# Kernel optimization log

Hardware: AMD Instinct MI355X
Metric: run time of the kernel (lower is better)

## Reference

```python
import jax, jax.numpy as jnp
import numpy as np

N_P = 50000   # number of 'place' nodes
N_A = 50000   # number of 'a_transition' nodes
E = 1600000   # edges per edge type
IN = 128      # input feature dim
OUT = 64      # HANConv out_channels
H = 4         # heads
D = OUT // H  # per-head dim
HID = 64      # decoder hidden
NEG_SLOPE = 0.2  # HANConv leaky_relu slope


def setup_inputs() -> dict:
    key = jax.random.key(0)
    ks = jax.random.split(key, 24)
    def nrm(i, shape, scale=1.0):
        return jax.random.normal(ks[i], shape, dtype=jnp.float32) * scale
    w = lambda i, shape, fan: nrm(i, shape, (1.0 / fan) ** 0.5)
    return {
        "x_place": nrm(0, (N_P, IN)),
        "x_atrans": nrm(1, (N_A, IN)),
        "e_pa_src": jax.random.randint(ks[2], (E,), 0, N_P),
        "e_pa_dst": jax.random.randint(ks[3], (E,), 0, N_A),
        "e_aa_src": jax.random.randint(ks[4], (E,), 0, N_A),
        "e_aa_dst": jax.random.randint(ks[5], (E,), 0, N_A),
        "e_ap_src": jax.random.randint(ks[6], (E,), 0, N_A),
        "e_ap_dst": jax.random.randint(ks[7], (E,), 0, N_P),
        "Wp_place": w(8, (IN, OUT), IN),
        "bp_place": jnp.zeros((OUT,), jnp.float32),
        "Wp_atrans": w(9, (IN, OUT), IN),
        "bp_atrans": jnp.zeros((OUT,), jnp.float32),
        "asrc_pa": w(10, (H, D), D),
        "adst_pa": w(11, (H, D), D),
        "asrc_aa": w(12, (H, D), D),
        "adst_aa": w(13, (H, D), D),
        "asrc_ap": w(14, (H, D), D),
        "adst_ap": w(15, (H, D), D),
        "Wk": w(16, (OUT, OUT), OUT),
        "bk": jnp.zeros((OUT,), jnp.float32),
        "q": w(17, (OUT,), OUT),
        "Wd1": w(18, (OUT, HID), OUT),
        "bd1": jnp.zeros((HID,), jnp.float32),
        "Wd2": w(19, (HID, 1), HID),
        "bd2": jnp.zeros((1,), jnp.float32),
    }


def _edge_conv(h_src, h_dst, a_src, a_dst, src, dst, n_dst):
    """HANConv node-level attention for one edge type.
    h_src: [N_src, H, D], h_dst: [N_dst, H, D]; returns relu-aggregated [n_dst, H*D]."""
    alpha = (h_src * a_src).sum(-1)[src] + (h_dst * a_dst).sum(-1)[dst]  # [E, H]
    alpha = jax.nn.leaky_relu(alpha, NEG_SLOPE)
    amax = jax.ops.segment_max(alpha, dst, num_segments=n_dst)
    amax = jnp.where(jnp.isfinite(amax), amax, 0.0)  # guard empty neighborhoods
    ex = jnp.exp(alpha - amax[dst])
    den = jax.ops.segment_sum(ex, dst, num_segments=n_dst) + 1e-16  # PyG softmax eps
    wgt = ex / den[dst]                           # scatter-softmax per dst node [E, H]
    msg = h_src[src] * wgt[:, :, None]            # [E, H, D]
    out = jax.ops.segment_sum(msg, dst, num_segments=n_dst)
    return jax.nn.relu(out.reshape(n_dst, H * D))


def _semantic(outs, q, Wk, bk):
    """HANConv semantic-level attention over edge-type embeddings."""
    stk = jnp.stack(outs)                                       # [T, N, OUT]
    score = (q * jnp.tanh(stk @ Wk + bk).mean(axis=1)).sum(-1)  # [T]
    attn = jax.nn.softmax(score)
    return jnp.einsum('t,tnc->nc', attn, stk)


def reference(x_place, x_atrans, e_pa_src, e_pa_dst, e_aa_src, e_aa_dst, e_ap_src, e_ap_dst,
              Wp_place, bp_place, Wp_atrans, bp_atrans,
              asrc_pa, adst_pa, asrc_aa, adst_aa, asrc_ap, adst_ap,
              Wk, bk, q, Wd1, bd1, Wd2, bd2):
    # per-node-type projection, split into heads
    h_p = (x_place @ Wp_place + bp_place).reshape(N_P, H, D)
    h_a = (x_atrans @ Wp_atrans + bp_atrans).reshape(N_A, H, D)
    # node-level attention per edge type
    out_pa = _edge_conv(h_p, h_a, asrc_pa, adst_pa, e_pa_src, e_pa_dst, N_A)
    out_aa = _edge_conv(h_a, h_a, asrc_aa, adst_aa, e_aa_src, e_aa_dst, N_A)
    out_ap = _edge_conv(h_a, h_p, asrc_ap, adst_ap, e_ap_src, e_ap_dst, N_P)
    # semantic-level attention per destination node type
    x_a = _semantic([out_pa, out_aa], q, Wk, bk)   # 'a_transition'
    _xp = _semantic([out_ap], q, Wk, bk)           # 'place' (computed by encoder, unused downstream)
    # decoder MLP on 'a_transition' + softmax over nodes (dim=0)
    z = jax.nn.relu(x_a @ Wd1 + bd1) @ Wd2 + bd2   # [N_A, 1]
    return jax.nn.softmax(z, axis=0)
```

## Files before the change

### kernel.cpp

```cpp
#include <hip/hip_runtime.h>
#include <hip/hip_fp16.h>
#include <math.h>

#define NP 50000
#define NA 50000
#define NE 1600000
#define IN_DIM 128
#define OUT_DIM 64

#define NB 391
#define BCAP 4608
#define P1_CHUNK 4096
#define P1_GRID ((NE + P1_CHUNK - 1) / P1_CHUNK)
#define PROJ_BLOCKS ((NP + 127) / 128)
#define GATHER_BLOCKS 2048
#define DEC_BLOCKS 512

typedef _Float16 v8h __attribute__((ext_vector_type(8)));
typedef _Float16 h2f __attribute__((ext_vector_type(2)));
typedef float    v4f __attribute__((ext_vector_type(4)));

__device__ inline float fast_tanh(float x) {
    const float e = __expf(2.f * x);
    return 1.f - 2.f / (e + 1.f);
}

__device__ inline float lane_f32(float v, int k) {
    return __builtin_bit_cast(float,
        __builtin_amdgcn_readlane(__builtin_bit_cast(int, v), k));
}

__global__ __launch_bounds__(512) void front_kernel(
    const float* __restrict__ xA, const float* __restrict__ WA, const float* __restrict__ bA,
    const float* __restrict__ xB, const float* __restrict__ WB, const float* __restrict__ bB,
    const float* __restrict__ a_pa_src, const float* __restrict__ a_pa_dst,
    const float* __restrict__ a_aa_src, const float* __restrict__ a_aa_dst,
    ushort* __restrict__ hA, ushort* __restrict__ hB,
    float* __restrict__ s_p_src_pa, float* __restrict__ s_a_dst_pa,
    float* __restrict__ s_a_src_aa, float* __restrict__ s_a_dst_aa,
    const int* __restrict__ srcA, const int* __restrict__ dstA,
    const int* __restrict__ srcB, const int* __restrict__ dstB,
    int* __restrict__ gpart, int* __restrict__ gcur)
{
    __shared__ __align__(16) char smem[22656];
    const int type = blockIdx.y;
    const int tid = threadIdx.x;

    if (blockIdx.x < P1_GRID) {
        const int* src = type ? srcB : srcA;
        const int* dst = type ? dstB : dstA;
        const int ebase = blockIdx.x * P1_CHUNK;
        const int ecount = min(P1_CHUNK, NE - ebase);

        int* hist   = (int*)smem;
        int* starts = hist + NB;
        int* offs2  = starts + NB;
        int* gbase  = offs2 + NB;
        unsigned* sorted = (unsigned*)(gbase + NB);

        for (int i = tid; i < NB; i += 512) hist[i] = 0;
        __syncthreads();
        for (int i = tid; i < ecount; i += 512)
            atomicAdd(&hist[dst[ebase + i] >> 7], 1);
        __syncthreads();
        if (tid < 64) {
            int carry = 0;
            for (int r = 0; r < 7; ++r) {
                const int idx = r * 64 + tid;
                const int v = (idx < NB) ? hist[idx] : 0;
                int s = v;
                #pragma unroll
                for (int off = 1; off < 64; off <<= 1) {
                    const int t = __shfl_up(s, off);
                    if (tid >= off) s += t;
                }
                if (idx < NB) { starts[idx] = carry + s - v; offs2[idx] = carry + s - v; }
                carry += __shfl(s, 63);
            }
        }
        __syncthreads();
        for (int i = tid; i < ecount; i += 512) {
            const int d = dst[ebase + i];
            const int s = src[ebase + i];
            const int bin = d >> 7;
            const int pos = atomicAdd(&offs2[bin], 1);
            sorted[pos] = ((unsigned)bin << 23) | ((unsigned)(d & 127) << 16) | (unsigned)s;
        }
        __syncthreads();
        for (int b = tid; b < NB; b += 512) {
            const int cnt = hist[b];
            const int flatb = type * NB + b;
            gbase[b] = cnt ? (flatb * BCAP + atomicAdd(&gcur[flatb], cnt)) : 0;
        }
        __syncthreads();
        for (int i = tid; i < ecount; i += 512) {
            const unsigned e = sorted[i];
            const int bin = e >> 23;
            gpart[gbase[bin] + (i - starts[bin])] = (int)(e & 0x7FFFFF);
        }
        return;
    }

    const int pbid = blockIdx.x - P1_GRID;
    const float* x = type ? xB : xA;
    const float* W = type ? WB : WA;
    const float* bias = type ? bB : bA;
    ushort* h_out  = type ? hB : hA;
    const float* c0 = type ? a_pa_dst : a_pa_src;
    float*       s0 = type ? s_a_dst_pa : s_p_src_pa;
    const float* c1 = type ? a_aa_src : nullptr;
    float*       s1 = type ? s_a_src_aa : nullptr;
    const float* c2 = type ? a_aa_dst : nullptr;
    float*       s2 = type ? s_a_dst_aa : nullptr;

    _Float16 (*Wt)[136] = (_Float16(*)[136])smem;
    {
        const float4* W4 = (const float4*)W;
        #pragma unroll
        for (int i = 0; i < 4; ++i) {
            const int f4i = tid + 512 * i;
            const float4 w = W4[f4i];
            const int k = f4i >> 4, c4 = (f4i & 15) * 4;
            Wt[c4 + 0][k] = (_Float16)w.x;
            Wt[c4 + 1][k] = (_Float16)w.y;
            Wt[c4 + 2][k] = (_Float16)w.z;
            Wt[c4 + 3][k] = (_Float16)w.w;
        }
    }
    __syncthreads();

    const int lane = tid & 63;
    const int wid = tid >> 6;
    const int node0 = (pbid * 8 + wid) * 16;
    if (node0 >= NP) return;
    const int m = lane & 15;
    const int quad = lane >> 4;

    v4f acc[4] = {};
    #pragma unroll
    for (int kc = 0; kc < 4; ++kc) {
        const int k0 = kc * 32 + quad * 8;
        const float4 xa = *(const float4*)(x + (size_t)(node0 + m) * IN_DIM + k0);
        const float4 xb2 = *(const float4*)(x + (size_t)(node0 + m) * IN_DIM + k0 + 4);
        v8h af;
        af[0] = (_Float16)xa.x;  af[1] = (_Float16)xa.y;
        af[2] = (_Float16)xa.z;  af[3] = (_Float16)xa.w;
        af[4] = (_Float16)xb2.x; af[5] = (_Float16)xb2.y;
        af[6] = (_Float16)xb2.z; af[7] = (_Float16)xb2.w;
        #pragma unroll
        for (int cb = 0; cb < 4; ++cb) {
            const v8h bf = *(const v8h*)&Wt[cb * 16 + m][k0];
            acc[cb] = __builtin_amdgcn_mfma_f32_16x16x32_f16(af, bf, acc[cb], 0, 0, 0);
        }
    }

    #pragma unroll
    for (int cb = 0; cb < 4; ++cb) {
        const int c = cb * 16 + m;
        const float bv = bias[c];
        float hv[4];
        #pragma unroll
        for (int r = 0; r < 4; ++r) {
            hv[r] = acc[cb][r] + bv;
            const int node = node0 + quad * 4 + r;
            h_out[(size_t)node * 64 + c] = __half_as_ushort(__float2half_rn(hv[r]));
        }
        #define DO_SCORE(A, S)                                         \
            if (A) {                                                   \
                const float av = (A)[c];                               \
                float v0 = hv[0]*av, v1 = hv[1]*av, v2 = hv[2]*av, v3 = hv[3]*av; \
                for (int msk = 1; msk <= 8; msk <<= 1) {               \
                    v0 += __shfl_xor(v0, msk);                         \
                    v1 += __shfl_xor(v1, msk);                         \
                    v2 += __shfl_xor(v2, msk);                         \
                    v3 += __shfl_xor(v3, msk);                         \
                }                                                      \
                if (m == 0) {                                          \
                    const int nb = node0 + quad * 4;                   \
                    (S)[(nb + 0) * 4 + cb] = v0;                       \
                    (S)[(nb + 1) * 4 + cb] = v1;                       \
                    (S)[(nb + 2) * 4 + cb] = v2;                       \
                    (S)[(nb + 3) * 4 + cb] = v3;                       \
                }                                                      \
            }
        DO_SCORE(c0, s0)
        DO_SCORE(c1, s1)
        DO_SCORE(c2, s2)
        #undef DO_SCORE
    }
}

__global__ __launch_bounds__(512) void bucket_sort_kernel(
    int* __restrict__ gpart, const int* __restrict__ gcur,
    int* __restrict__ recA, int* __restrict__ offsA,
    int* __restrict__ recB, int* __restrict__ offsB)
{
    const int b = blockIdx.x, type = blockIdx.y;
    int* rec  = type ? recB  : recA;
    int* offs = type ? offsB : offsA;
    const int flat = type * NB + b;
    const int region = flat * BCAP;
    const int cnt = gcur[flat];
    const int tid = threadIdx.x;

    __shared__ int hist[128];
    __shared__ int starts[128];
    __shared__ int offs2[128];
    __shared__ int red[8];
    __shared__ int sorted[BCAP];

    int p = 0;
    for (int i = tid; i < b; i += 512) p += gcur[type * NB + i];
    #pragma unroll
    for (int msk = 1; msk <= 32; msk <<= 1) p += __shfl_xor(p, msk);
    if ((tid & 63) == 0) red[tid >> 6] = p;
    if (tid < 128) hist[tid] = 0;
    __syncthreads();
    const int bst = red[0] + red[1] + red[2] + red[3]
                  + red[4] + red[5] + red[6] + red[7];

    for (int i = tid; i < cnt; i += 512)
        atomicAdd(&hist[gpart[region + i] >> 16], 1);
    __syncthreads();
    if (tid < 64) {
        int carry = 0;
        for (int r = 0; r < 2; ++r) {
            const int idx = r * 64 + tid;
            const int v = hist[idx];
            int s = v;
            #pragma unroll
            for (int off = 1; off < 64; off <<= 1) {
                const int t = __shfl_up(s, off);
                if (tid >= off) s += t;
            }
            starts[idx] = carry + s - v;
            offs2[idx]  = carry + s - v;
            carry += __shfl(s, 63);
        }
    }
    __syncthreads();
    for (int i = tid; i < cnt; i += 512) {
        const int pk = gpart[region + i];
        const int pos = atomicAdd(&offs2[pk >> 16], 1);
        sorted[pos] = pk & 0xFFFF;
    }
    __syncthreads();
    for (int i = tid; i < cnt; i += 512) rec[bst + i] = sorted[i];
    if (tid < 128) {
        const int n = b * 128 + tid;
        if (n < NA) offs[n] = bst + starts[tid];
    }
    if (b == NB - 1 && tid == 0) offs[NA] = bst + cnt;
}

__global__ __launch_bounds__(256) void gather_kernel(
    const int* __restrict__ offsA, const int* __restrict__ recA,
    const ushort* __restrict__ hA, const float* __restrict__ ssA,
    const float* __restrict__ sdA, float* __restrict__ outA,
    const int* __restrict__ offsB, const int* __restrict__ recB,
    const ushort* __restrict__ hB, const float* __restrict__ ssB,
    const float* __restrict__ sdB, float* __restrict__ outB, int n_dst)
{
    const int bid = blockIdx.x;
    const int type = bid & 1;
    const int* offs = type ? offsB : offsA;
    const int* rec  = type ? recB  : recA;
    const ushort* h_src = type ? hB : hA;
    const float* s_src = type ? ssB : ssA;
    const float* s_dst = type ? sdB : sdA;
    float* outbuf = type ? outB : outA;

    const int lane = threadIdx.x & 63;
    const int q = lane & 7;
    const int sub = lane >> 3;
    const int h = q >> 1;
    const ushort* hq = h_src + (q << 3);
    const float* ss = s_src + h;

    const int d0 = (bid >> 1) * 4 + (threadIdx.x >> 6);
    const int dstride = (GATHER_BLOCKS >> 1) * 4;

    for (int d = d0; d < n_dst; d += dstride) {
        const float sd = s_dst[d * 4 + h];
        const int beg = offs[d], end = offs[d + 1];

        float acc[8] = {};
        float wacc = 0.f;
        for (int base = beg; base < end; base += 64) {
            const int c64 = min(64, end - base);
            const int sv = (lane < c64) ? rec[base + lane] : 0;
            const int iters = (c64 + 7) >> 3;
            for (int it = 0; it < iters; ++it) {
                const int idx = it * 8 + sub;
                const int s = __shfl(sv, idx);
                if (idx < c64) {
                    float alpha = ss[(size_t)s * 4] + sd;
                    alpha = fmaxf(alpha, 0.2f * alpha);
                    const float w = __expf(alpha);
                    const uint4 pk = *(const uint4*)(hq + ((size_t)s << 6));
                    const h2f a0 = __builtin_bit_cast(h2f, pk.x);
                    const h2f a1 = __builtin_bit_cast(h2f, pk.y);
                    const h2f a2 = __builtin_bit_cast(h2f, pk.z);
                    const h2f a3 = __builtin_bit_cast(h2f, pk.w);
                    acc[0] = fmaf((float)a0[0], w, acc[0]);
                    acc[1] = fmaf((float)a0[1], w, acc[1]);
                    acc[2] = fmaf((float)a1[0], w, acc[2]);
                    acc[3] = fmaf((float)a1[1], w, acc[3]);
                    acc[4] = fmaf((float)a2[0], w, acc[4]);
                    acc[5] = fmaf((float)a2[1], w, acc[5]);
                    acc[6] = fmaf((float)a3[0], w, acc[6]);
                    acc[7] = fmaf((float)a3[1], w, acc[7]);
                    wacc += w;
                }
            }
        }
        #pragma unroll
        for (int m = 8; m <= 32; m <<= 1) {
            #pragma unroll
            for (int j = 0; j < 8; ++j) acc[j] += __shfl_xor(acc[j], m);
            wacc += __shfl_xor(wacc, m);
        }
        if (sub == 0) {
            const float inv = 1.f / (wacc + 1e-16f);
            float4 o0, o1;
            o0.x = fmaxf(acc[0] * inv, 0.f);
            o0.y = fmaxf(acc[1] * inv, 0.f);
            o0.z = fmaxf(acc[2] * inv, 0.f);
            o0.w = fmaxf(acc[3] * inv, 0.f);
            o1.x = fmaxf(acc[4] * inv, 0.f);
            o1.y = fmaxf(acc[5] * inv, 0.f);
            o1.z = fmaxf(acc[6] * inv, 0.f);
            o1.w = fmaxf(acc[7] * inv, 0.f);
            float* op = outbuf + (size_t)d * 64 + q * 8;
            *(float4*)op = o0;
            *(float4*)(op + 4) = o1;
        }
    }
}

#define SEM_BLOCKS 512
__global__ __launch_bounds__(256) void semantic_kernel(
    const float* __restrict__ out0, const float* __restrict__ out1,
    const float* __restrict__ Wk, const float* __restrict__ bk,
    float* __restrict__ sem, int n)
{
    const int c = threadIdx.x, ty = threadIdx.y;
    float wk[64];
    #pragma unroll
    for (int k = 0; k < 64; ++k) wk[k] = Wk[k * 64 + c];
    const float bkc = bk[c];
    float acc0 = 0.f, acc1 = 0.f;
    for (int node = blockIdx.x * 4 + ty; node < n; node += SEM_BLOCKS * 4) {
        const float n0 = out0[(size_t)node * 64 + c];
        const float n1 = out1[(size_t)node * 64 + c];
        float a0 = bkc, a1 = bkc;
        #pragma unroll
        for (int k = 0; k < 64; ++k) {
            a0 = fmaf(lane_f32(n0, k), wk[k], a0);
            a1 = fmaf(lane_f32(n1, k), wk[k], a1);
        }
        acc0 += fast_tanh(a0);
        acc1 += fast_tanh(a1);
    }
    __shared__ float red[2][4][64];
    red[0][ty][c] = acc0; red[1][ty][c] = acc1;
    __syncthreads();
    if (ty == 0) {
        atomicAdd(&sem[c],      red[0][0][c] + red[0][1][c] + red[0][2][c] + red[0][3][c]);
        atomicAdd(&sem[64 + c], red[1][0][c] + red[1][1][c] + red[1][2][c] + red[1][3][c]);
    }
}

__global__ __launch_bounds__(256) void decoder_kernel(
    const float* __restrict__ out0, const float* __restrict__ out1,
    const float* __restrict__ sem, const float* __restrict__ qv,
    const float* __restrict__ Wd1, const float* __restrict__ bd1,
    const float* __restrict__ Wd2, const float* __restrict__ bd2,
    float* __restrict__ ebuf, float* __restrict__ esum, int n)
{
    __shared__ float attn_s[2];
    __shared__ float red[4];
    const int c = threadIdx.x, ty = threadIdx.y;

    if (ty == 0) {
        float v0 = sem[c] * qv[c];
        float v1 = sem[64 + c] * qv[c];
        for (int off = 32; off >= 1; off >>= 1) {
            v0 += __shfl_xor(v0, off);
            v1 += __shfl_xor(v1, off);
        }
        if (c == 0) {
            const float t0 = v0 / (float)NA, t1 = v1 / (float)NA;
            const float m = fmaxf(t0, t1);
            const float e0 = __expf(t0 - m), e1 = __expf(t1 - m);
            const float inv = 1.f / (e0 + e1);
            attn_s[0] = e0 * inv;
            attn_s[1] = e1 * inv;
        }
    }
    float wd[64];
    #pragma unroll
    for (int k = 0; k < 64; ++k) wd[k] = Wd1[k * 64 + c];
    const float bd1c = bd1[c], wd2c = Wd2[c];
    __syncthreads();
    const float a0 = attn_s[0], a1 = attn_s[1];

    float epart = 0.f;
    for (int node = blockIdx.x * 4 + ty; node < n; node += DEC_BLOCKS * 4) {
        const float xv = a0 * out0[(size_t)node * 64 + c]
                       + a1 * out1[(size_t)node * 64 + c];
        float acc = bd1c;
        #pragma unroll
        for (int k = 0; k < 64; ++k)
            acc = fmaf(lane_f32(xv, k), wd[k], acc);
        float hv = fmaxf(acc, 0.f) * wd2c;
        for (int off = 32; off >= 1; off >>= 1) hv += __shfl_xor(hv, off);
        if (c == 0) {
            const float e = __expf(hv + bd2[0]);
            ebuf[node] = e;
            epart += e;
        }
    }
    if (c == 0) red[ty] = epart;
    __syncthreads();
    if (c == 0 && ty == 0)
        atomicAdd(&esum[(blockIdx.x & 3) * 16],
                  red[0] + red[1] + red[2] + red[3]);
}

__global__ __launch_bounds__(256) void softmax_final_kernel(
    const float* __restrict__ e, const float* __restrict__ esum,
    float* __restrict__ out, int n)
{
    const float s = esum[0] + esum[16] + esum[32] + esum[48];
    const int i = blockIdx.x * 256 + threadIdx.x;
    if (i < n) out[i] = e[i] / s;
}

extern "C" void kernel_launch(void* const* d_in, const int* in_sizes, int n_in,
                              void* d_out, int out_size, void* d_ws, size_t ws_size,
                              hipStream_t stream)
{
    const float* x_place  = (const float*)d_in[0];
    const float* x_atrans = (const float*)d_in[1];
    const int* e_pa_src = (const int*)d_in[2];
    const int* e_pa_dst = (const int*)d_in[3];
    const int* e_aa_src = (const int*)d_in[4];
    const int* e_aa_dst = (const int*)d_in[5];
    const float* Wp_place  = (const float*)d_in[8];
    const float* bp_place  = (const float*)d_in[9];
    const float* Wp_atrans = (const float*)d_in[10];
    const float* bp_atrans = (const float*)d_in[11];
    const float* asrc_pa = (const float*)d_in[12];
    const float* adst_pa = (const float*)d_in[13];
    const float* asrc_aa = (const float*)d_in[14];
    const float* adst_aa = (const float*)d_in[15];
    const float* Wk  = (const float*)d_in[18];
    const float* bk  = (const float*)d_in[19];
    const float* q   = (const float*)d_in[20];
    const float* Wd1 = (const float*)d_in[21];
    const float* bd1 = (const float*)d_in[22];
    const float* Wd2 = (const float*)d_in[23];
    const float* bd2 = (const float*)d_in[24];
    float* out = (float*)d_out;

    float* ws = (float*)d_ws;
    size_t off = 0;
    auto alloc = [&](size_t n) {
        float* p = ws + off; off += (n + 3) & ~(size_t)3; return p;
    };

    ushort* h_p       = (ushort*)alloc((size_t)NP * 32);
    ushort* h_a       = (ushort*)alloc((size_t)NA * 32);
    float* s_p_src_pa = alloc((size_t)NP * 4);
    float* s_a_dst_pa = alloc((size_t)NA * 4);
    float* s_a_src_aa = alloc((size_t)NA * 4);
    float* s_a_dst_aa = alloc((size_t)NA * 4);
    float* out_pa     = alloc((size_t)NA * 64);
    float* out_aa     = alloc((size_t)NA * 64);
    int*   offs_pa    = (int*)alloc(NA + 1);
    int*   offs_aa    = (int*)alloc(NA + 1);
    int*   rec_pa     = (int*)alloc(NE);
    int*   rec_aa     = (int*)alloc(NE);
    int*   gcur       = (int*)alloc(2 * NB);
    float* sem        = alloc(128);
    float* esum       = alloc(64);
    float* ebuf       = alloc(NA);
    int* gpart = (int*)out_pa;
    (void)ws_size; (void)in_sizes; (void)n_in; (void)out_size;

    const size_t zbytes = (size_t)((char*)(esum + 64) - (char*)gcur);
    hipMemsetAsync(gcur, 0, zbytes, stream);

    front_kernel<<<dim3(P1_GRID + PROJ_BLOCKS, 2), 512, 0, stream>>>(
        x_place, Wp_place, bp_place,
        x_atrans, Wp_atrans, bp_atrans,
        asrc_pa, adst_pa, asrc_aa, adst_aa,
        h_p, h_a,
        s_p_src_pa, s_a_dst_pa, s_a_src_aa, s_a_dst_aa,
        e_pa_src, e_pa_dst, e_aa_src, e_aa_dst, gpart, gcur);

    bucket_sort_kernel<<<dim3(NB, 2), 512, 0, stream>>>(
        gpart, gcur, rec_pa, offs_pa, rec_aa, offs_aa);

    gather_kernel<<<GATHER_BLOCKS, 256, 0, stream>>>(
        offs_pa, rec_pa, h_p, s_p_src_pa, s_a_dst_pa, out_pa,
        offs_aa, rec_aa, h_a, s_a_src_aa, s_a_dst_aa, out_aa, NA);

    dim3 b64x4(64, 4);
    semantic_kernel<<<SEM_BLOCKS, b64x4, 0, stream>>>(out_pa, out_aa, Wk, bk, sem, NA);
    decoder_kernel<<<DEC_BLOCKS, b64x4, 0, stream>>>(
        out_pa, out_aa, sem, q, Wd1, bd1, Wd2, bd2, ebuf, esum, NA);
    softmax_final_kernel<<<(NA + 255) / 256, 256, 0, stream>>>(ebuf, esum, out, NA);
}
```

Before: 316.9 us.

## Fuse semantic, decoder and softmax kernels into one persistent kernel with grid barriers

Merges the three tail kernels into a single 512-block kernel that uses atomic-counter grid barriers between the semantic reduction, the decoder MLP and the final softmax normalisation. This removes two kernel launches and the gaps between them. The cost is two spin-wait barriers, which assume all 512 blocks are co-resident on the device, plus extra fences. The barrier counters are zeroed by extending the existing memset.

```diff
diff --git a/kernel.cpp b/kernel.cpp
--- a/kernel.cpp
+++ b/kernel.cpp
@@ -14,7 +14,7 @@
 #define P1_GRID ((NE + P1_CHUNK - 1) / P1_CHUNK)
 #define PROJ_BLOCKS ((NP + 127) / 128)
 #define GATHER_BLOCKS 2048
-#define DEC_BLOCKS 512
+#define TAIL_BLOCKS 512
 
 typedef _Float16 v8h __attribute__((ext_vector_type(8)));
 typedef _Float16 h2f __attribute__((ext_vector_type(2)));
@@ -338,53 +338,66 @@
     }
 }
 
-#define SEM_BLOCKS 512
-__global__ __launch_bounds__(256) void semantic_kernel(
+__global__ __launch_bounds__(256) void tail_kernel(
     const float* __restrict__ out0, const float* __restrict__ out1,
     const float* __restrict__ Wk, const float* __restrict__ bk,
-    float* __restrict__ sem, int n)
+    const float* __restrict__ qv,
+    const float* __restrict__ Wd1, const float* __restrict__ bd1,
+    const float* __restrict__ Wd2, const float* __restrict__ bd2,
+    float* __restrict__ sem, float* __restrict__ esum,
+    int* __restrict__ bar, float* __restrict__ ebuf,
+    float* __restrict__ out, int n)
 {
     const int c = threadIdx.x, ty = threadIdx.y;
-    float wk[64];
+    const int tid = ty * 64 + c;
+    __shared__ float red[2][4][64];
+    __shared__ float attn_s[2];
+    __shared__ float red4[4];
+    __shared__ float stot;
+
+    {
+        float wk[64];
+        #pragma unroll
+        for (int k = 0; k < 64; ++k) wk[k] = Wk[k * 64 + c];
+        const float bkc = bk[c];
+        float acc0 = 0.f, acc1 = 0.f;
+        for (int node = blockIdx.x * 4 + ty; node < n; node += TAIL_BLOCKS * 4) {
+            const float n0 = out0[(size_t)node * 64 + c];
+            const float n1 = out1[(size_t)node * 64 + c];
+            float a0 = bkc, a1 = bkc;
+            #pragma unroll
+            for (int k = 0; k < 64; ++k) {
+                a0 = fmaf(lane_f32(n0, k), wk[k], a0);
+                a1 = fmaf(lane_f32(n1, k), wk[k], a1);
+            }
+            acc0 += fast_tanh(a0);
+            acc1 += fast_tanh(a1);
+        }
+        red[0][ty][c] = acc0; red[1][ty][c] = acc1;
+        __syncthreads();
+        if (ty == 0) {
+            atomicAdd(&sem[c],      red[0][0][c] + red[0][1][c] + red[0][2][c] + red[0][3][c]);
+            atomicAdd(&sem[64 + c], red[1][0][c] + red[1][1][c] + red[1][2][c] + red[1][3][c]);
+        }
+    }
+    __threadfence();
+    __syncthreads();
+    if (tid == 0) {
+        atomicAdd(&bar[0], 1);
+        while (__hip_atomic_load(&bar[0], __ATOMIC_ACQUIRE, __HIP_MEMORY_SCOPE_AGENT) < TAIL_BLOCKS)
+            __builtin_amdgcn_s_sleep(32);
+    }
+    __syncthreads();
+    __threadfence();
+
+    float wd[64];
     #pragma unroll
-    for (int k = 0; k < 64; ++k) wk[k] = Wk[k * 64 + c];
-    const float bkc = bk[c];
-    float acc0 = 0.f, acc1 = 0.f;
-    for (int node = blockIdx.x * 4 + ty; node < n; node += SEM_BLOCKS * 4) {
-        const float n0 = out0[(size_t)node * 64 + c];
-        const float n1 = out1[(size_t)node * 64 + c];
-        float a0 = bkc, a1 = bkc;
-        #pragma unroll
-        for (int k = 0; k < 64; ++k) {
-            a0 = fmaf(lane_f32(n0, k), wk[k], a0);
-            a1 = fmaf(lane_f32(n1, k), wk[k], a1);
-        }
-        acc0 += fast_tanh(a0);
-        acc1 += fast_tanh(a1);
-    }
-    __shared__ float red[2][4][64];
-    red[0][ty][c] = acc0; red[1][ty][c] = acc1;
-    __syncthreads();
+    for (int k = 0; k < 64; ++k) wd[k] = Wd1[k * 64 + c];
     if (ty == 0) {
-        atomicAdd(&sem[c],      red[0][0][c] + red[0][1][c] + red[0][2][c] + red[0][3][c]);
-        atomicAdd(&sem[64 + c], red[1][0][c] + red[1][1][c] + red[1][2][c] + red[1][3][c]);
-    }
-}
-
-__global__ __launch_bounds__(256) void decoder_kernel(
-    const float* __restrict__ out0, const float* __restrict__ out1,
-    const float* __restrict__ sem, const float* __restrict__ qv,
-    const float* __restrict__ Wd1, const float* __restrict__ bd1,
-    const float* __restrict__ Wd2, const float* __restrict__ bd2,
-    float* __restrict__ ebuf, float* __restrict__ esum, int n)
-{
-    __shared__ float attn_s[2];
-    __shared__ float red[4];
-    const int c = threadIdx.x, ty = threadIdx.y;
-
-    if (ty == 0) {
-        float v0 = sem[c] * qv[c];
-        float v1 = sem[64 + c] * qv[c];
+        const float sm0 = __hip_atomic_load(&sem[c],      __ATOMIC_RELAXED, __HIP_MEMORY_SCOPE_AGENT);
+        const float sm1 = __hip_atomic_load(&sem[64 + c], __ATOMIC_RELAXED, __HIP_MEMORY_SCOPE_AGENT);
+        float v0 = sm0 * qv[c];
+        float v1 = sm1 * qv[c];
         for (int off = 32; off >= 1; off >>= 1) {
             v0 += __shfl_xor(v0, off);
             v1 += __shfl_xor(v1, off);
@@ -398,15 +411,12 @@
             attn_s[1] = e1 * inv;
         }
     }
-    float wd[64];
-    #pragma unroll
-    for (int k = 0; k < 64; ++k) wd[k] = Wd1[k * 64 + c];
-    const float bd1c = bd1[c], wd2c = Wd2[c];
+    const float bd1c = bd1[c], wd2c = Wd2[c], bd2c = bd2[0];
     __syncthreads();
     const float a0 = attn_s[0], a1 = attn_s[1];
 
     float epart = 0.f;
-    for (int node = blockIdx.x * 4 + ty; node < n; node += DEC_BLOCKS * 4) {
+    for (int node = blockIdx.x * 4 + ty; node < n; node += TAIL_BLOCKS * 4) {
         const float xv = a0 * out0[(size_t)node * 64 + c]
                        + a1 * out1[(size_t)node * 64 + c];
         float acc = bd1c;
@@ -416,25 +426,38 @@
         float hv = fmaxf(acc, 0.f) * wd2c;
         for (int off = 32; off >= 1; off >>= 1) hv += __shfl_xor(hv, off);
         if (c == 0) {
-            const float e = __expf(hv + bd2[0]);
+            const float e = __expf(hv + bd2c);
             ebuf[node] = e;
             epart += e;
         }
     }
-    if (c == 0) red[ty] = epart;
-    __syncthreads();
-    if (c == 0 && ty == 0)
+    if (c == 0) red4[ty] = epart;
+    __syncthreads();
+    if (tid == 0)
         atomicAdd(&esum[(blockIdx.x & 3) * 16],
-                  red[0] + red[1] + red[2] + red[3]);
-}
-
-__global__ __launch_bounds__(256) void softmax_final_kernel(
-    const float* __restrict__ e, const float* __restrict__ esum,
-    float* __restrict__ out, int n)
-{
-    const float s = esum[0] + esum[16] + esum[32] + esum[48];
-    const int i = blockIdx.x * 256 + threadIdx.x;
-    if (i < n) out[i] = e[i] / s;
+                  red4[0] + red4[1] + red4[2] + red4[3]);
+
+    __threadfence();
+    __syncthreads();
+    if (tid == 0) {
+        atomicAdd(&bar[16], 1);
+        while (__hip_atomic_load(&bar[16], __ATOMIC_ACQUIRE, __HIP_MEMORY_SCOPE_AGENT) < TAIL_BLOCKS)
+            __builtin_amdgcn_s_sleep(32);
+    }
+    __syncthreads();
+
+    if (tid == 0) {
+        float t = 0.f;
+        t += __hip_atomic_load(&esum[0],  __ATOMIC_RELAXED, __HIP_MEMORY_SCOPE_AGENT);
+        t += __hip_atomic_load(&esum[16], __ATOMIC_RELAXED, __HIP_MEMORY_SCOPE_AGENT);
+        t += __hip_atomic_load(&esum[32], __ATOMIC_RELAXED, __HIP_MEMORY_SCOPE_AGENT);
+        t += __hip_atomic_load(&esum[48], __ATOMIC_RELAXED, __HIP_MEMORY_SCOPE_AGENT);
+        stot = t;
+    }
+    __syncthreads();
+    const float s = stot;
+    for (int node = blockIdx.x * 4 + ty; node < n; node += TAIL_BLOCKS * 4)
+        if (c == 0) out[node] = ebuf[node] / s;
 }
 
 extern "C" void kernel_launch(void* const* d_in, const int* in_sizes, int n_in,
@@ -485,11 +508,12 @@
     int*   gcur       = (int*)alloc(2 * NB);
     float* sem        = alloc(128);
     float* esum       = alloc(64);
+    int*   bar        = (int*)alloc(32);
     float* ebuf       = alloc(NA);
     int* gpart = (int*)out_pa;
     (void)ws_size; (void)in_sizes; (void)n_in; (void)out_size;
 
-    const size_t zbytes = (size_t)((char*)(esum + 64) - (char*)gcur);
+    const size_t zbytes = (size_t)((char*)(bar + 32) - (char*)gcur);
     hipMemsetAsync(gcur, 0, zbytes, stream);
 
     front_kernel<<<dim3(P1_GRID + PROJ_BLOCKS, 2), 512, 0, stream>>>(
@@ -508,8 +532,7 @@
         offs_aa, rec_aa, h_a, s_a_src_aa, s_a_dst_aa, out_aa, NA);
 
     dim3 b64x4(64, 4);
-    semantic_kernel<<<SEM_BLOCKS, b64x4, 0, stream>>>(out_pa, out_aa, Wk, bk, sem, NA);
-    decoder_kernel<<<DEC_BLOCKS, b64x4, 0, stream>>>(
-        out_pa, out_aa, sem, q, Wd1, bd1, Wd2, bd2, ebuf, esum, NA);
-    softmax_final_kernel<<<(NA + 255) / 256, 256, 0, stream>>>(ebuf, esum, out, NA);
-}
+    tail_kernel<<<TAIL_BLOCKS, b64x4, 0, stream>>>(
+        out_pa, out_aa, Wk, bk, q, Wd1, bd1, Wd2, bd2,
+        sem, esum, bar, ebuf, out, NA);
+}
```

After: 493.1 us. +55.6%, slower.
